# Performance work log

Measured on AMD Instinct MI355X. Metric: run time of the kernel, lower is better.

Reference implementation:

```python
import jax, jax.numpy as jnp
import numpy as np

N_NODES = 100000


def _gcn_conv(x, src, dst, deg_inv_sqrt, W, b, num_nodes):
    # GCNConv: out = D^{-1/2} (A+I) D^{-1/2} (x W) + b, with self-loops already
    # appended to (src, dst) and deg_inv_sqrt precomputed over the augmented graph.
    h = x @ W                                            # [N, out]
    coef = deg_inv_sqrt[src] * deg_inv_sqrt[dst]         # [E+N]
    msg = h[src] * coef[:, None]                         # gather + normalize
    out = jax.ops.segment_sum(msg, dst, num_segments=num_nodes)  # scatter-add
    return out + b


def setup_inputs() -> dict:
    key = jax.random.key(0)
    ks = jax.random.split(key, 8)
    n, d, h = N_NODES, 16, 16
    E = 3_200_000
    x = jax.random.normal(ks[0], (n, d), dtype=jnp.float32)
    edge_index = jax.random.randint(ks[1], (2, E), 0, n, dtype=jnp.int64)
    # Glorot-ish init for weights, zeros for biases (as in GCNConv/Linear defaults)
    W1 = jax.random.normal(ks[2], (d, h), dtype=jnp.float32) / np.sqrt(d)
    b1 = jnp.zeros((h,), dtype=jnp.float32)
    W2 = jax.random.normal(ks[3], (h, h), dtype=jnp.float32) / np.sqrt(h)
    b2 = jnp.zeros((h,), dtype=jnp.float32)
    Wfc = jax.random.normal(ks[4], (h, 1), dtype=jnp.float32) / np.sqrt(h)
    bfc = jnp.zeros((1,), dtype=jnp.float32)
    return {"x": x, "edge_index": edge_index, "W1": W1, "b1": b1,
            "W2": W2, "b2": b2, "Wfc": Wfc, "bfc": bfc}


def reference(x, edge_index, W1, b1, W2, b2, Wfc, bfc):
    n = x.shape[0]
    loops = jnp.arange(n, dtype=edge_index.dtype)
    src = jnp.concatenate([edge_index[0], loops])
    dst = jnp.concatenate([edge_index[1], loops])
    # symmetric normalization over graph with self-loops (edge weight 1)
    deg = jax.ops.segment_sum(jnp.ones_like(dst, dtype=x.dtype), dst, num_segments=n)
    deg_inv_sqrt = jnp.where(deg > 0, jax.lax.rsqrt(deg), 0.0)
    h = jax.nn.relu(_gcn_conv(x, src, dst, deg_inv_sqrt, W1, b1, n))
    h = jax.nn.relu(_gcn_conv(h, src, dst, deg_inv_sqrt, W2, b2, n))
    return h @ Wfc + bfc  # [N, 1]
```

## Files before the change

### kernel.cpp

```cpp
#include <hip/hip_runtime.h>
#include <hip/hip_fp16.h>
#include <stdint.h>


constexpr int F = 16;
constexpr int K_MAX = 256;
constexpr int BNODES = 512;
constexpr int PT = 4096;
constexpr int NPB = 128;
constexpr unsigned int CAP = 18432;

__global__ void ginit_kernel(unsigned int* __restrict__ gcur, int K) {
    int i = threadIdx.x;
    if (i < K) gcur[i] = (unsigned int)i * CAP;
}

__global__ void __launch_bounds__(256)
partition_kernel(const int* __restrict__ src, const int* __restrict__ dst,
                 unsigned int* __restrict__ gcur, unsigned int* __restrict__ recs,
                 int E, int K) {
    __shared__ unsigned int hist[K_MAX];
    __shared__ unsigned int offs[K_MAX];
    __shared__ unsigned int gbase[K_MAX];
    __shared__ unsigned int drec[PT];
    __shared__ unsigned char dbuk[PT];
    const int t = threadIdx.x;
    const int tile0 = blockIdx.x * PT;
    const int cnt = min(PT, E - tile0);
    if (t < K) hist[t] = 0u;
    __syncthreads();
    unsigned int rec[16], bp[16];
#pragma unroll
    for (int k = 0; k < 16; ++k) {
        int i = t + k * 256;
        bp[k] = 0xFFFFFFFFu;
        if (i < cnt) {
            int e = tile0 + i;
            unsigned int d = (unsigned int)dst[e];
            unsigned int s = (unsigned int)src[e];
            unsigned int b = d >> 9;
            rec[k] = ((d & 511u) << 17) | s;
            unsigned int pos = atomicAdd(&hist[b], 1u);
            bp[k] = (b << 12) | pos;
        }
    }
    __syncthreads();
    if (t < K) gbase[t] = atomicAdd(&gcur[t], hist[t]);
    if (t == 0) {
        unsigned int run = 0;
        for (int i = 0; i < K; ++i) { offs[i] = run; run += hist[i]; }
    }
    __syncthreads();
#pragma unroll
    for (int k = 0; k < 16; ++k) {
        if (bp[k] != 0xFFFFFFFFu) {
            unsigned int b = bp[k] >> 12, pos = bp[k] & 0xFFFu;
            unsigned int idx = offs[b] + pos;
            drec[idx] = rec[k];
            dbuk[idx] = (unsigned char)b;
        }
    }
    __syncthreads();
    for (int i = t; i < cnt; i += 256) {
        unsigned int b = dbuk[i];
        recs[gbase[b] + ((unsigned int)i - offs[b])] = drec[i];
    }
}

__global__ void __launch_bounds__(512)
sort_kernel(const unsigned int* __restrict__ recs, const unsigned int* __restrict__ gcur,
            float* __restrict__ dis, unsigned int* __restrict__ rp,
            unsigned int* __restrict__ recs2, int N) {
    __shared__ unsigned int cur[BNODES];
    __shared__ unsigned int wsum[8];
    const int b = blockIdx.x;
    const int t = threadIdx.x;
    const int lane = t & 63, wid = t >> 6;
    cur[t] = 0u;
    __syncthreads();
    const unsigned int e0 = (unsigned int)b * CAP;
    const unsigned int e1 = gcur[b];
    for (unsigned int e = e0 + t; e < e1; e += 512)
        atomicAdd(&cur[recs[e] >> 17], 1u);
    __syncthreads();
    const unsigned int c = cur[t];
    unsigned int x = c;
#pragma unroll
    for (int o = 1; o < 64; o <<= 1) {
        unsigned int y = __shfl_up(x, o, 64);
        if (lane >= o) x += y;
    }
    if (lane == 63) wsum[wid] = x;
    __syncthreads();
    if (t == 0) {
        unsigned int run = 0;
#pragma unroll
        for (int i = 0; i < 8; ++i) { unsigned int tmp = wsum[i]; wsum[i] = run; run += tmp; }
    }
    __syncthreads();
    const unsigned int start = e0 + wsum[wid] + x - c;
    const int v = b * BNODES + t;
    if (v < N) {
        dis[v] = rsqrtf(1.0f + (float)c);
        rp[v] = (c << 24) | start;
    }
    __syncthreads();
    cur[t] = start;
    __syncthreads();
    for (unsigned int e = e0 + t; e < e1; e += 512) {
        unsigned int r = recs[e];
        unsigned int slot = atomicAdd(&cur[r >> 17], 1u);
        recs2[slot] = r & 0x1FFFFu;
    }
}

__global__ void mv_scale_kernel(const float* __restrict__ x, const float* __restrict__ W,
                                const float* __restrict__ dis, __half* __restrict__ hs, int N) {
    __shared__ float xs[16][17];
    __shared__ float ws[16][16];
    int tid = threadIdx.x;
    int n = tid >> 4, j = tid & 15;
    int node = blockIdx.x * 16 + n;
    ws[n][j] = W[tid];
    xs[n][j] = (node < N) ? x[node * F + j] : 0.0f;
    __syncthreads();
    float acc = 0.f;
#pragma unroll
    for (int k = 0; k < 16; ++k) acc += xs[n][k] * ws[k][j];
    if (node < N) hs[node * F + j] = __float2half(acc * dis[node]);
}

__device__ __forceinline__ float2 h2f2(__half2 h) { return __half22float2(h); }

__global__ void __launch_bounds__(256)
agg1_kernel(const unsigned int* __restrict__ recs2, const unsigned int* __restrict__ rp,
            const __half2* __restrict__ hs1, const float* __restrict__ dis,
            const float* __restrict__ W2, const float* __restrict__ b1,
            __half* __restrict__ hs2, int N) {
    __shared__ float ws[16][16];
    __shared__ float hbf[NPB][17];
    const int t = threadIdx.x;
    ws[t >> 4][t & 15] = W2[t];
    const int j2 = t & 7;
    const int g8 = t >> 3;
    const int v0 = blockIdx.x * NPB;
#pragma unroll
    for (int it = 0; it < 4; ++it) {
        const int n = g8 + 32 * it;
        const int v = v0 + n;
        float sx = 0.f, sy = 0.f;
        float dv = 0.f;
        if (v < N) {
            dv = dis[v];
            const unsigned int w = rp[v];
            unsigned int e = w & 0xFFFFFFu;
            const unsigned int e1 = e + (w >> 24);
            float2 s = h2f2(hs1[(size_t)v * 8 + j2]);
            sx = s.x; sy = s.y;
            for (; e + 8 <= e1; e += 8) {
                unsigned int r0 = recs2[e + 0], r1 = recs2[e + 1];
                unsigned int r2 = recs2[e + 2], r3 = recs2[e + 3];
                unsigned int r4 = recs2[e + 4], r5 = recs2[e + 5];
                unsigned int r6 = recs2[e + 6], r7 = recs2[e + 7];
                float2 a0 = h2f2(hs1[r0 * 8 + j2]), a1 = h2f2(hs1[r1 * 8 + j2]);
                float2 a2 = h2f2(hs1[r2 * 8 + j2]), a3 = h2f2(hs1[r3 * 8 + j2]);
                float2 a4 = h2f2(hs1[r4 * 8 + j2]), a5 = h2f2(hs1[r5 * 8 + j2]);
                float2 a6 = h2f2(hs1[r6 * 8 + j2]), a7 = h2f2(hs1[r7 * 8 + j2]);
                sx += ((a0.x + a1.x) + (a2.x + a3.x)) + ((a4.x + a5.x) + (a6.x + a7.x));
                sy += ((a0.y + a1.y) + (a2.y + a3.y)) + ((a4.y + a5.y) + (a6.y + a7.y));
            }
            for (; e < e1; ++e) {
                float2 a = h2f2(hs1[recs2[e] * 8 + j2]);
                sx += a.x; sy += a.y;
            }
        }
        hbf[n][2 * j2 + 0] = fmaxf(dv * sx + b1[2 * j2 + 0], 0.f);
        hbf[n][2 * j2 + 1] = fmaxf(dv * sy + b1[2 * j2 + 1], 0.f);
    }
    __syncthreads();
    const int j = t & 15;
    const int g = t >> 4;
#pragma unroll
    for (int it = 0; it < 8; ++it) {
        const int n = g + 16 * it;
        const int v = v0 + n;
        if (v >= N) continue;
        float acc = 0.f;
#pragma unroll
        for (int k = 0; k < 16; ++k) acc += hbf[n][k] * ws[k][j];
        hs2[(size_t)v * F + j] = __float2half(acc * dis[v]);
    }
}

__global__ void __launch_bounds__(256)
agg2_kernel(const unsigned int* __restrict__ recs2, const unsigned int* __restrict__ rp,
            const __half2* __restrict__ hs2, const float* __restrict__ dis,
            const float* __restrict__ b2, const float* __restrict__ Wfc,
            const float* __restrict__ bfc, float* __restrict__ out, int N) {
    const int t = threadIdx.x;
    const int j2 = t & 7;
    const int g8 = t >> 3;
    const int v0 = blockIdx.x * NPB;
    const float wfx = Wfc[2 * j2 + 0], wfy = Wfc[2 * j2 + 1];
    const float bbx = b2[2 * j2 + 0], bby = b2[2 * j2 + 1];
    const float bf = bfc[0];
#pragma unroll
    for (int it = 0; it < 4; ++it) {
        const int v = v0 + g8 + 32 * it;
        if (v >= N) continue;
        const unsigned int w = rp[v];
        unsigned int e = w & 0xFFFFFFu;
        const unsigned int e1 = e + (w >> 24);
        float2 s0 = h2f2(hs2[(size_t)v * 8 + j2]);
        float sx = s0.x, sy = s0.y;
        for (; e + 8 <= e1; e += 8) {
            unsigned int r0 = recs2[e + 0], r1 = recs2[e + 1];
            unsigned int r2 = recs2[e + 2], r3 = recs2[e + 3];
            unsigned int r4 = recs2[e + 4], r5 = recs2[e + 5];
            unsigned int r6 = recs2[e + 6], r7 = recs2[e + 7];
            float2 a0 = h2f2(hs2[r0 * 8 + j2]), a1 = h2f2(hs2[r1 * 8 + j2]);
            float2 a2 = h2f2(hs2[r2 * 8 + j2]), a3 = h2f2(hs2[r3 * 8 + j2]);
            float2 a4 = h2f2(hs2[r4 * 8 + j2]), a5 = h2f2(hs2[r5 * 8 + j2]);
            float2 a6 = h2f2(hs2[r6 * 8 + j2]), a7 = h2f2(hs2[r7 * 8 + j2]);
            sx += ((a0.x + a1.x) + (a2.x + a3.x)) + ((a4.x + a5.x) + (a6.x + a7.x));
            sy += ((a0.y + a1.y) + (a2.y + a3.y)) + ((a4.y + a5.y) + (a6.y + a7.y));
        }
        for (; e < e1; ++e) {
            float2 a = h2f2(hs2[recs2[e] * 8 + j2]);
            sx += a.x; sy += a.y;
        }
        const float dv = dis[v];
        float h = fmaxf(dv * sx + bbx, 0.f) * wfx + fmaxf(dv * sy + bby, 0.f) * wfy;
        h += __shfl_down(h, 4, 8);
        h += __shfl_down(h, 2, 8);
        h += __shfl_down(h, 1, 8);
        if (j2 == 0) out[v] = h + bf;
    }
}

static inline char* align256(char* p) {
    return (char*)(((uintptr_t)p + 255) & ~(uintptr_t)255);
}

extern "C" void kernel_launch(void* const* d_in, const int* in_sizes, int n_in,
                              void* d_out, int out_size, void* d_ws, size_t ws_size,
                              hipStream_t stream) {
    const float* x   = (const float*)d_in[0];
    const int*   ei  = (const int*)d_in[1];
    const float* W1  = (const float*)d_in[2];
    const float* b1  = (const float*)d_in[3];
    const float* W2  = (const float*)d_in[4];
    const float* b2  = (const float*)d_in[5];
    const float* Wfc = (const float*)d_in[6];
    const float* bfc = (const float*)d_in[7];
    float* out = (float*)d_out;

    const int N = in_sizes[0] / F;
    const int E = in_sizes[1] / 2;
    const int* src = ei;
    const int* dst = ei + E;

    const int K = (N + BNODES - 1) / BNODES;

    char* p = (char*)d_ws;
    float* dis = (float*)align256(p);                   p = (char*)(dis + N);
    unsigned int* gcur  = (unsigned int*)align256(p);   p = (char*)(gcur + K);
    unsigned int* rp    = (unsigned int*)align256(p);   p = (char*)(rp + N);
    unsigned int* recs2 = (unsigned int*)align256(p);   p = (char*)(recs2 + (size_t)K * CAP);
    unsigned int* recs  = (unsigned int*)align256(p);
    __half* hs1 = (__half*)recs;
    __half* hs2 = hs1 + (size_t)N * F;

    const int T = 256;

    ginit_kernel<<<1, T, 0, stream>>>(gcur, K);
    partition_kernel<<<(E + PT - 1) / PT, T, 0, stream>>>(src, dst, gcur, recs, E, K);
    sort_kernel<<<K, 512, 0, stream>>>(recs, gcur, dis, rp, recs2, N);
    mv_scale_kernel<<<(N + 15) / 16, T, 0, stream>>>(x, W1, dis, hs1, N);
    agg1_kernel<<<(N + NPB - 1) / NPB, T, 0, stream>>>(recs2, rp, (const __half2*)hs1, dis, W2, b1, hs2, N);
    agg2_kernel<<<(N + NPB - 1) / NPB, T, 0, stream>>>(recs2, rp, (const __half2*)hs2, dis, b2, Wfc, bfc, out, N);
}
```

Before: 209.3 us.

## Fuse all GCN stages into one cooperative persistent kernel with grid syncs

Replaces the six separate launches (init, partition, sort, transform, two aggregations) with one cooperative persistent kernel that loops over tiles and separates phases with grid.sync, sharing a unioned shared-memory buffer. The partition tile is halved so each tile fits the shared-memory union under the occupancy bound. The goal is to remove launch gaps and tail effects between the small kernels. In exchange it pays for grid-wide barriers, may get lower occupancy, and the sort phase now uses 256 threads per bucket instead of 512. The old multi-kernel path remains as a fallback if the cooperative launch fails.

```diff
diff --git a/kernel.cpp b/kernel.cpp
--- a/kernel.cpp
+++ b/kernel.cpp
@@ -1,14 +1,271 @@
 #include <hip/hip_runtime.h>
 #include <hip/hip_fp16.h>
+#include <hip/hip_cooperative_groups.h>
 #include <stdint.h>
+
+namespace cg = cooperative_groups;
 
 
 constexpr int F = 16;
 constexpr int K_MAX = 256;
 constexpr int BNODES = 512;
-constexpr int PT = 4096;
+constexpr int PT = 2048;
 constexpr int NPB = 128;
 constexpr unsigned int CAP = 18432;
+
+struct SU {
+    union {
+        struct {
+            unsigned int hist[K_MAX], offs[K_MAX], gbase[K_MAX];
+            unsigned int drec[PT];
+            unsigned char dbuk[PT];
+        } part;
+        struct { unsigned int cur[BNODES]; unsigned int wsum[4]; } sort;
+        struct { float ws[16][16]; float xs[16][17]; } mv;
+        struct { float ws[16][16]; float hbf[NPB][17]; } agg;
+    };
+};
+
+__device__ __forceinline__ float2 h2f2(__half2 h) { return __half22float2(h); }
+
+__global__ void __launch_bounds__(256, 4)
+fused_kernel(const int* __restrict__ src, const int* __restrict__ dst,
+             const float* __restrict__ x,
+             const float* __restrict__ W1, const float* __restrict__ b1,
+             const float* __restrict__ W2, const float* __restrict__ b2,
+             const float* __restrict__ Wfc, const float* __restrict__ bfc,
+             float* __restrict__ out,
+             unsigned int* __restrict__ gcur, unsigned int* __restrict__ rp,
+             unsigned int* __restrict__ recs, unsigned int* __restrict__ recs2,
+             float* __restrict__ dis, __half* __restrict__ hs1, __half* __restrict__ hs2,
+             int N, int E, int K) {
+    __shared__ SU su;
+    cg::grid_group grid = cg::this_grid();
+    const int t = threadIdx.x;
+    const int blk = blockIdx.x;
+    const int nblk = gridDim.x;
+
+    {
+        int gid = blk * 256 + t;
+        if (gid < K) gcur[gid] = (unsigned int)gid * CAP;
+    }
+    grid.sync();
+
+    {
+        const int ntiles = (E + PT - 1) / PT;
+        for (int tile = blk; tile < ntiles; tile += nblk) {
+            const int tile0 = tile * PT;
+            const int cnt = min(PT, E - tile0);
+            if (t < K) su.part.hist[t] = 0u;
+            __syncthreads();
+            unsigned int rec[8], bp[8];
+#pragma unroll
+            for (int k = 0; k < 8; ++k) {
+                int i = t + k * 256;
+                bp[k] = 0xFFFFFFFFu;
+                if (i < cnt) {
+                    int e = tile0 + i;
+                    unsigned int d = (unsigned int)dst[e];
+                    unsigned int s = (unsigned int)src[e];
+                    unsigned int b = d >> 9;
+                    rec[k] = ((d & 511u) << 17) | s;
+                    unsigned int pos = atomicAdd(&su.part.hist[b], 1u);
+                    bp[k] = (b << 12) | pos;
+                }
+            }
+            __syncthreads();
+            if (t < K) su.part.gbase[t] = atomicAdd(&gcur[t], su.part.hist[t]);
+            if (t == 0) {
+                unsigned int run = 0;
+                for (int i = 0; i < K; ++i) { su.part.offs[i] = run; run += su.part.hist[i]; }
+            }
+            __syncthreads();
+#pragma unroll
+            for (int k = 0; k < 8; ++k) {
+                if (bp[k] != 0xFFFFFFFFu) {
+                    unsigned int b = bp[k] >> 12, pos = bp[k] & 0xFFFu;
+                    unsigned int idx = su.part.offs[b] + pos;
+                    su.part.drec[idx] = rec[k];
+                    su.part.dbuk[idx] = (unsigned char)b;
+                }
+            }
+            __syncthreads();
+            for (int i = t; i < cnt; i += 256) {
+                unsigned int b = su.part.dbuk[i];
+                recs[su.part.gbase[b] + ((unsigned int)i - su.part.offs[b])] = su.part.drec[i];
+            }
+            __syncthreads();
+        }
+    }
+    grid.sync();
+
+    {
+        const int lane = t & 63, wid = t >> 6;
+        for (int b = blk; b < K; b += nblk) {
+            su.sort.cur[2 * t] = 0u;
+            su.sort.cur[2 * t + 1] = 0u;
+            __syncthreads();
+            const unsigned int e0 = (unsigned int)b * CAP;
+            const unsigned int e1 = gcur[b];
+            for (unsigned int e = e0 + t; e < e1; e += 256)
+                atomicAdd(&su.sort.cur[recs[e] >> 17], 1u);
+            __syncthreads();
+            const unsigned int c0 = su.sort.cur[2 * t];
+            const unsigned int c1 = su.sort.cur[2 * t + 1];
+            const unsigned int loc = c0 + c1;
+            unsigned int xs = loc;
+#pragma unroll
+            for (int o = 1; o < 64; o <<= 1) {
+                unsigned int y = __shfl_up(xs, o, 64);
+                if (lane >= o) xs += y;
+            }
+            if (lane == 63) su.sort.wsum[wid] = xs;
+            __syncthreads();
+            if (t == 0) {
+                unsigned int run = 0;
+#pragma unroll
+                for (int i = 0; i < 4; ++i) { unsigned int tmp = su.sort.wsum[i]; su.sort.wsum[i] = run; run += tmp; }
+            }
+            __syncthreads();
+            const unsigned int start0 = e0 + su.sort.wsum[wid] + xs - loc;
+            const unsigned int start1 = start0 + c0;
+            const int v0 = b * BNODES + 2 * t;
+            if (v0 < N)     { dis[v0] = rsqrtf(1.0f + (float)c0); rp[v0] = (c0 << 24) | start0; }
+            if (v0 + 1 < N) { dis[v0 + 1] = rsqrtf(1.0f + (float)c1); rp[v0 + 1] = (c1 << 24) | start1; }
+            __syncthreads();
+            su.sort.cur[2 * t] = start0;
+            su.sort.cur[2 * t + 1] = start1;
+            __syncthreads();
+            for (unsigned int e = e0 + t; e < e1; e += 256) {
+                unsigned int r = recs[e];
+                unsigned int slot = atomicAdd(&su.sort.cur[r >> 17], 1u);
+                recs2[slot] = r & 0x1FFFFu;
+            }
+            __syncthreads();
+        }
+    }
+    grid.sync();
+
+    {
+        const int n = t >> 4, j = t & 15;
+        su.mv.ws[n][j] = W1[t];
+        __syncthreads();
+        const int ntiles = (N + 15) / 16;
+        for (int tile = blk; tile < ntiles; tile += nblk) {
+            const int node = tile * 16 + n;
+            su.mv.xs[n][j] = (node < N) ? x[node * F + j] : 0.0f;
+            __syncthreads();
+            float acc = 0.f;
+#pragma unroll
+            for (int k = 0; k < 16; ++k) acc += su.mv.xs[n][k] * su.mv.ws[k][j];
+            if (node < N) hs1[node * F + j] = __float2half(acc * dis[node]);
+            __syncthreads();
+        }
+    }
+    grid.sync();
+
+    {
+        const int j = t & 15, g = t >> 4;
+        su.agg.ws[g][j] = W2[t];
+        __syncthreads();
+        const __half2* h1 = (const __half2*)hs1;
+        const int j2 = t & 7, g8 = t >> 3;
+        const int nchunks = (N + NPB - 1) / NPB;
+        for (int chunk = blk; chunk < nchunks; chunk += nblk) {
+            const int v0 = chunk * NPB;
+#pragma unroll
+            for (int it = 0; it < 4; ++it) {
+                const int n = g8 + 32 * it;
+                const int v = v0 + n;
+                float sx = 0.f, sy = 0.f, dv = 0.f;
+                if (v < N) {
+                    dv = dis[v];
+                    const unsigned int w = rp[v];
+                    unsigned int e = w & 0xFFFFFFu;
+                    const unsigned int e1 = e + (w >> 24);
+                    float2 s = h2f2(h1[(size_t)v * 8 + j2]);
+                    sx = s.x; sy = s.y;
+                    for (; e + 8 <= e1; e += 8) {
+                        unsigned int r0 = recs2[e + 0], r1 = recs2[e + 1];
+                        unsigned int r2 = recs2[e + 2], r3 = recs2[e + 3];
+                        unsigned int r4 = recs2[e + 4], r5 = recs2[e + 5];
+                        unsigned int r6 = recs2[e + 6], r7 = recs2[e + 7];
+                        float2 a0 = h2f2(h1[r0 * 8 + j2]), a1 = h2f2(h1[r1 * 8 + j2]);
+                        float2 a2 = h2f2(h1[r2 * 8 + j2]), a3 = h2f2(h1[r3 * 8 + j2]);
+                        float2 a4 = h2f2(h1[r4 * 8 + j2]), a5 = h2f2(h1[r5 * 8 + j2]);
+                        float2 a6 = h2f2(h1[r6 * 8 + j2]), a7 = h2f2(h1[r7 * 8 + j2]);
+                        sx += ((a0.x + a1.x) + (a2.x + a3.x)) + ((a4.x + a5.x) + (a6.x + a7.x));
+                        sy += ((a0.y + a1.y) + (a2.y + a3.y)) + ((a4.y + a5.y) + (a6.y + a7.y));
+                    }
+                    for (; e < e1; ++e) {
+                        float2 a = h2f2(h1[recs2[e] * 8 + j2]);
+                        sx += a.x; sy += a.y;
+                    }
+                }
+                su.agg.hbf[n][2 * j2 + 0] = fmaxf(dv * sx + b1[2 * j2 + 0], 0.f);
+                su.agg.hbf[n][2 * j2 + 1] = fmaxf(dv * sy + b1[2 * j2 + 1], 0.f);
+            }
+            __syncthreads();
+#pragma unroll
+            for (int it = 0; it < 8; ++it) {
+                const int n = g + 16 * it;
+                const int v = v0 + n;
+                if (v < N) {
+                    float acc = 0.f;
+#pragma unroll
+                    for (int k = 0; k < 16; ++k) acc += su.agg.hbf[n][k] * su.agg.ws[k][j];
+                    hs2[(size_t)v * F + j] = __float2half(acc * dis[v]);
+                }
+            }
+            __syncthreads();
+        }
+    }
+    grid.sync();
+
+    {
+        const __half2* h2 = (const __half2*)hs2;
+        const int j2 = t & 7, g8 = t >> 3;
+        const float wfx = Wfc[2 * j2 + 0], wfy = Wfc[2 * j2 + 1];
+        const float bbx = b2[2 * j2 + 0], bby = b2[2 * j2 + 1];
+        const float bf = bfc[0];
+        const int nchunks = (N + NPB - 1) / NPB;
+        for (int chunk = blk; chunk < nchunks; chunk += nblk) {
+            const int v0 = chunk * NPB;
+#pragma unroll
+            for (int it = 0; it < 4; ++it) {
+                const int v = v0 + g8 + 32 * it;
+                if (v >= N) continue;
+                const unsigned int w = rp[v];
+                unsigned int e = w & 0xFFFFFFu;
+                const unsigned int e1 = e + (w >> 24);
+                float2 s0 = h2f2(h2[(size_t)v * 8 + j2]);
+                float sx = s0.x, sy = s0.y;
+                for (; e + 8 <= e1; e += 8) {
+                    unsigned int r0 = recs2[e + 0], r1 = recs2[e + 1];
+                    unsigned int r2 = recs2[e + 2], r3 = recs2[e + 3];
+                    unsigned int r4 = recs2[e + 4], r5 = recs2[e + 5];
+                    unsigned int r6 = recs2[e + 6], r7 = recs2[e + 7];
+                    float2 a0 = h2f2(h2[r0 * 8 + j2]), a1 = h2f2(h2[r1 * 8 + j2]);
+                    float2 a2 = h2f2(h2[r2 * 8 + j2]), a3 = h2f2(h2[r3 * 8 + j2]);
+                    float2 a4 = h2f2(h2[r4 * 8 + j2]), a5 = h2f2(h2[r5 * 8 + j2]);
+                    float2 a6 = h2f2(h2[r6 * 8 + j2]), a7 = h2f2(h2[r7 * 8 + j2]);
+                    sx += ((a0.x + a1.x) + (a2.x + a3.x)) + ((a4.x + a5.x) + (a6.x + a7.x));
+                    sy += ((a0.y + a1.y) + (a2.y + a3.y)) + ((a4.y + a5.y) + (a6.y + a7.y));
+                }
+                for (; e < e1; ++e) {
+                    float2 a = h2f2(h2[recs2[e] * 8 + j2]);
+                    sx += a.x; sy += a.y;
+                }
+                const float dv = dis[v];
+                float h = fmaxf(dv * sx + bbx, 0.f) * wfx + fmaxf(dv * sy + bby, 0.f) * wfy;
+                h += __shfl_down(h, 4, 8);
+                h += __shfl_down(h, 2, 8);
+                h += __shfl_down(h, 1, 8);
+                if (j2 == 0) out[v] = h + bf;
+            }
+        }
+    }
+}
 
 __global__ void ginit_kernel(unsigned int* __restrict__ gcur, int K) {
     int i = threadIdx.x;
@@ -29,9 +286,9 @@
     const int cnt = min(PT, E - tile0);
     if (t < K) hist[t] = 0u;
     __syncthreads();
-    unsigned int rec[16], bp[16];
-#pragma unroll
-    for (int k = 0; k < 16; ++k) {
+    unsigned int rec[8], bp[8];
+#pragma unroll
+    for (int k = 0; k < 8; ++k) {
         int i = t + k * 256;
         bp[k] = 0xFFFFFFFFu;
         if (i < cnt) {
@@ -52,7 +309,7 @@
     }
     __syncthreads();
 #pragma unroll
-    for (int k = 0; k < 16; ++k) {
+    for (int k = 0; k < 8; ++k) {
         if (bp[k] != 0xFFFFFFFFu) {
             unsigned int b = bp[k] >> 12, pos = bp[k] & 0xFFFu;
             unsigned int idx = offs[b] + pos;
@@ -129,8 +386,6 @@
     for (int k = 0; k < 16; ++k) acc += xs[n][k] * ws[k][j];
     if (node < N) hs[node * F + j] = __float2half(acc * dis[node]);
 }
-
-__device__ __forceinline__ float2 h2f2(__half2 h) { return __half22float2(h); }
 
 __global__ void __launch_bounds__(256)
 agg1_kernel(const unsigned int* __restrict__ recs2, const unsigned int* __restrict__ rp,
@@ -148,8 +403,7 @@
     for (int it = 0; it < 4; ++it) {
         const int n = g8 + 32 * it;
         const int v = v0 + n;
-        float sx = 0.f, sy = 0.f;
-        float dv = 0.f;
+        float sx = 0.f, sy = 0.f, dv = 0.f;
         if (v < N) {
             dv = dis[v];
             const unsigned int w = rp[v];
@@ -255,12 +509,11 @@
     const float* bfc = (const float*)d_in[7];
     float* out = (float*)d_out;
 
-    const int N = in_sizes[0] / F;
-    const int E = in_sizes[1] / 2;
+    int N = in_sizes[0] / F;
+    int E = in_sizes[1] / 2;
     const int* src = ei;
     const int* dst = ei + E;
-
-    const int K = (N + BNODES - 1) / BNODES;
+    int K = (N + BNODES - 1) / BNODES;
 
     char* p = (char*)d_ws;
     float* dis = (float*)align256(p);                   p = (char*)(dis + N);
@@ -271,12 +524,24 @@
     __half* hs1 = (__half*)recs;
     __half* hs2 = hs1 + (size_t)N * F;
 
-    const int T = 256;
-
-    ginit_kernel<<<1, T, 0, stream>>>(gcur, K);
-    partition_kernel<<<(E + PT - 1) / PT, T, 0, stream>>>(src, dst, gcur, recs, E, K);
-    sort_kernel<<<K, 512, 0, stream>>>(recs, gcur, dis, rp, recs2, N);
-    mv_scale_kernel<<<(N + 15) / 16, T, 0, stream>>>(x, W1, dis, hs1, N);
-    agg1_kernel<<<(N + NPB - 1) / NPB, T, 0, stream>>>(recs2, rp, (const __half2*)hs1, dis, W2, b1, hs2, N);
-    agg2_kernel<<<(N + NPB - 1) / NPB, T, 0, stream>>>(recs2, rp, (const __half2*)hs2, dis, b2, Wfc, bfc, out, N);
-}
+    int nb = 0;
+    hipError_t qerr = hipOccupancyMaxActiveBlocksPerMultiprocessor(
+        &nb, (const void*)fused_kernel, 256, 0);
+    hipError_t lerr = hipErrorUnknown;
+    if (qerr == hipSuccess && nb > 0) {
+        int grid = nb * 256;
+        void* args[] = { &src, &dst, &x, &W1, &b1, &W2, &b2, &Wfc, &bfc, &out,
+                         &gcur, &rp, &recs, &recs2, &dis, &hs1, &hs2, &N, &E, &K };
+        lerr = hipLaunchCooperativeKernel((void*)fused_kernel, dim3(grid),
+                                          dim3(256), args, 0, stream);
+    }
+    if (lerr != hipSuccess) {
+        const int T = 256;
+        ginit_kernel<<<1, T, 0, stream>>>(gcur, K);
+        partition_kernel<<<(E + PT - 1) / PT, T, 0, stream>>>(src, dst, gcur, recs, E, K);
+        sort_kernel<<<K, 512, 0, stream>>>(recs, gcur, dis, rp, recs2, N);
+        mv_scale_kernel<<<(N + 15) / 16, T, 0, stream>>>(x, W1, dis, hs1, N);
+        agg1_kernel<<<(N + NPB - 1) / NPB, T, 0, stream>>>(recs2, rp, (const __half2*)hs1, dis, W2, b1, hs2, N);
+        agg2_kernel<<<(N + NPB - 1) / NPB, T, 0, stream>>>(recs2, rp, (const __half2*)hs2, dis, b2, Wfc, bfc, out, N);
+    }
+}
```

After: 650.4 us. 211% more time.

## Fuse first-layer matvec into sort kernel and shrink aggregation node blocks

Applied to the files above, without the earlier changes.

Folds the first-layer x·W1 scaled by the degree norm into the per-bucket sort kernel, reusing the degree values already in shared memory, so a separate launch and its dis reread go away. The gcur init kernel becomes a memset, with the bucket base offset added inside the partition and sort kernels. The aggregation kernels now handle 32 nodes per block instead of 128, giving more blocks and better load balance for the irregular gather. hs1/hs2 get their own buffers instead of aliasing recs. The sort blocks do more serial work, and smaller agg blocks lose per-block reuse of the W2 load.

```diff
diff --git a/kernel.cpp b/kernel.cpp
--- a/kernel.cpp
+++ b/kernel.cpp
@@ -7,13 +7,10 @@
 constexpr int K_MAX = 256;
 constexpr int BNODES = 512;
 constexpr int PT = 4096;
-constexpr int NPB = 128;
+constexpr int NPB = 32;
 constexpr unsigned int CAP = 18432;
 
-__global__ void ginit_kernel(unsigned int* __restrict__ gcur, int K) {
-    int i = threadIdx.x;
-    if (i < K) gcur[i] = (unsigned int)i * CAP;
-}
+__device__ __forceinline__ float2 h2f2(__half2 h) { return __half22float2(h); }
 
 __global__ void __launch_bounds__(256)
 partition_kernel(const int* __restrict__ src, const int* __restrict__ dst,
@@ -45,7 +42,7 @@
         }
     }
     __syncthreads();
-    if (t < K) gbase[t] = atomicAdd(&gcur[t], hist[t]);
+    if (t < K) gbase[t] = (unsigned int)t * CAP + atomicAdd(&gcur[t], hist[t]);
     if (t == 0) {
         unsigned int run = 0;
         for (int i = 0; i < K; ++i) { offs[i] = run; run += hist[i]; }
@@ -68,29 +65,34 @@
 }
 
 __global__ void __launch_bounds__(512)
-sort_kernel(const unsigned int* __restrict__ recs, const unsigned int* __restrict__ gcur,
-            float* __restrict__ dis, unsigned int* __restrict__ rp,
-            unsigned int* __restrict__ recs2, int N) {
+sort_mv_kernel(const unsigned int* __restrict__ recs, const unsigned int* __restrict__ gcur,
+               const float* __restrict__ x, const float* __restrict__ W1,
+               float* __restrict__ dis, unsigned int* __restrict__ rp,
+               unsigned int* __restrict__ recs2, __half* __restrict__ hs1, int N) {
     __shared__ unsigned int cur[BNODES];
     __shared__ unsigned int wsum[8];
+    __shared__ float sdis[BNODES];
+    __shared__ float ws[16][16];
+    __shared__ float xs[32][17];
     const int b = blockIdx.x;
     const int t = threadIdx.x;
     const int lane = t & 63, wid = t >> 6;
     cur[t] = 0u;
+    if (t < 256) ws[t >> 4][t & 15] = W1[t];
     __syncthreads();
     const unsigned int e0 = (unsigned int)b * CAP;
-    const unsigned int e1 = gcur[b];
+    const unsigned int e1 = e0 + gcur[b];
     for (unsigned int e = e0 + t; e < e1; e += 512)
         atomicAdd(&cur[recs[e] >> 17], 1u);
     __syncthreads();
     const unsigned int c = cur[t];
-    unsigned int x = c;
+    unsigned int xsc = c;
 #pragma unroll
     for (int o = 1; o < 64; o <<= 1) {
-        unsigned int y = __shfl_up(x, o, 64);
-        if (lane >= o) x += y;
-    }
-    if (lane == 63) wsum[wid] = x;
+        unsigned int y = __shfl_up(xsc, o, 64);
+        if (lane >= o) xsc += y;
+    }
+    if (lane == 63) wsum[wid] = xsc;
     __syncthreads();
     if (t == 0) {
         unsigned int run = 0;
@@ -98,10 +100,12 @@
         for (int i = 0; i < 8; ++i) { unsigned int tmp = wsum[i]; wsum[i] = run; run += tmp; }
     }
     __syncthreads();
-    const unsigned int start = e0 + wsum[wid] + x - c;
+    const unsigned int start = e0 + wsum[wid] + xsc - c;
     const int v = b * BNODES + t;
+    const float dv = rsqrtf(1.0f + (float)c);
+    sdis[t] = dv;
     if (v < N) {
-        dis[v] = rsqrtf(1.0f + (float)c);
+        dis[v] = dv;
         rp[v] = (c << 24) | start;
     }
     __syncthreads();
@@ -112,25 +116,20 @@
         unsigned int slot = atomicAdd(&cur[r >> 17], 1u);
         recs2[slot] = r & 0x1FFFFu;
     }
-}
-
-__global__ void mv_scale_kernel(const float* __restrict__ x, const float* __restrict__ W,
-                                const float* __restrict__ dis, __half* __restrict__ hs, int N) {
-    __shared__ float xs[16][17];
-    __shared__ float ws[16][16];
-    int tid = threadIdx.x;
-    int n = tid >> 4, j = tid & 15;
-    int node = blockIdx.x * 16 + n;
-    ws[n][j] = W[tid];
-    xs[n][j] = (node < N) ? x[node * F + j] : 0.0f;
-    __syncthreads();
-    float acc = 0.f;
-#pragma unroll
-    for (int k = 0; k < 16; ++k) acc += xs[n][k] * ws[k][j];
-    if (node < N) hs[node * F + j] = __float2half(acc * dis[node]);
-}
-
-__device__ __forceinline__ float2 h2f2(__half2 h) { return __half22float2(h); }
+    const int n = t >> 4, j = t & 15;
+#pragma unroll
+    for (int tile = 0; tile < 16; ++tile) {
+        const int loc = tile * 32 + n;
+        const int node = b * BNODES + loc;
+        __syncthreads();
+        xs[n][j] = (node < N) ? x[(size_t)node * F + j] : 0.0f;
+        __syncthreads();
+        float acc = 0.f;
+#pragma unroll
+        for (int k = 0; k < 16; ++k) acc += xs[n][k] * ws[k][j];
+        if (node < N) hs1[(size_t)node * F + j] = __float2half(acc * sdis[loc]);
+    }
+}
 
 __global__ void __launch_bounds__(256)
 agg1_kernel(const unsigned int* __restrict__ recs2, const unsigned int* __restrict__ rp,
@@ -144,12 +143,9 @@
     const int j2 = t & 7;
     const int g8 = t >> 3;
     const int v0 = blockIdx.x * NPB;
-#pragma unroll
-    for (int it = 0; it < 4; ++it) {
-        const int n = g8 + 32 * it;
-        const int v = v0 + n;
-        float sx = 0.f, sy = 0.f;
-        float dv = 0.f;
+    {
+        const int v = v0 + g8;
+        float sx = 0.f, sy = 0.f, dv = 0.f;
         if (v < N) {
             dv = dis[v];
             const unsigned int w = rp[v];
@@ -174,14 +170,14 @@
                 sx += a.x; sy += a.y;
             }
         }
-        hbf[n][2 * j2 + 0] = fmaxf(dv * sx + b1[2 * j2 + 0], 0.f);
-        hbf[n][2 * j2 + 1] = fmaxf(dv * sy + b1[2 * j2 + 1], 0.f);
+        hbf[g8][2 * j2 + 0] = fmaxf(dv * sx + b1[2 * j2 + 0], 0.f);
+        hbf[g8][2 * j2 + 1] = fmaxf(dv * sy + b1[2 * j2 + 1], 0.f);
     }
     __syncthreads();
     const int j = t & 15;
     const int g = t >> 4;
 #pragma unroll
-    for (int it = 0; it < 8; ++it) {
+    for (int it = 0; it < 2; ++it) {
         const int n = g + 16 * it;
         const int v = v0 + n;
         if (v >= N) continue;
@@ -204,38 +200,35 @@
     const float wfx = Wfc[2 * j2 + 0], wfy = Wfc[2 * j2 + 1];
     const float bbx = b2[2 * j2 + 0], bby = b2[2 * j2 + 1];
     const float bf = bfc[0];
-#pragma unroll
-    for (int it = 0; it < 4; ++it) {
-        const int v = v0 + g8 + 32 * it;
-        if (v >= N) continue;
-        const unsigned int w = rp[v];
-        unsigned int e = w & 0xFFFFFFu;
-        const unsigned int e1 = e + (w >> 24);
-        float2 s0 = h2f2(hs2[(size_t)v * 8 + j2]);
-        float sx = s0.x, sy = s0.y;
-        for (; e + 8 <= e1; e += 8) {
-            unsigned int r0 = recs2[e + 0], r1 = recs2[e + 1];
-            unsigned int r2 = recs2[e + 2], r3 = recs2[e + 3];
-            unsigned int r4 = recs2[e + 4], r5 = recs2[e + 5];
-            unsigned int r6 = recs2[e + 6], r7 = recs2[e + 7];
-            float2 a0 = h2f2(hs2[r0 * 8 + j2]), a1 = h2f2(hs2[r1 * 8 + j2]);
-            float2 a2 = h2f2(hs2[r2 * 8 + j2]), a3 = h2f2(hs2[r3 * 8 + j2]);
-            float2 a4 = h2f2(hs2[r4 * 8 + j2]), a5 = h2f2(hs2[r5 * 8 + j2]);
-            float2 a6 = h2f2(hs2[r6 * 8 + j2]), a7 = h2f2(hs2[r7 * 8 + j2]);
-            sx += ((a0.x + a1.x) + (a2.x + a3.x)) + ((a4.x + a5.x) + (a6.x + a7.x));
-            sy += ((a0.y + a1.y) + (a2.y + a3.y)) + ((a4.y + a5.y) + (a6.y + a7.y));
-        }
-        for (; e < e1; ++e) {
-            float2 a = h2f2(hs2[recs2[e] * 8 + j2]);
-            sx += a.x; sy += a.y;
-        }
-        const float dv = dis[v];
-        float h = fmaxf(dv * sx + bbx, 0.f) * wfx + fmaxf(dv * sy + bby, 0.f) * wfy;
-        h += __shfl_down(h, 4, 8);
-        h += __shfl_down(h, 2, 8);
-        h += __shfl_down(h, 1, 8);
-        if (j2 == 0) out[v] = h + bf;
-    }
+    const int v = v0 + g8;
+    if (v >= N) return;
+    const unsigned int w = rp[v];
+    unsigned int e = w & 0xFFFFFFu;
+    const unsigned int e1 = e + (w >> 24);
+    float2 s0 = h2f2(hs2[(size_t)v * 8 + j2]);
+    float sx = s0.x, sy = s0.y;
+    for (; e + 8 <= e1; e += 8) {
+        unsigned int r0 = recs2[e + 0], r1 = recs2[e + 1];
+        unsigned int r2 = recs2[e + 2], r3 = recs2[e + 3];
+        unsigned int r4 = recs2[e + 4], r5 = recs2[e + 5];
+        unsigned int r6 = recs2[e + 6], r7 = recs2[e + 7];
+        float2 a0 = h2f2(hs2[r0 * 8 + j2]), a1 = h2f2(hs2[r1 * 8 + j2]);
+        float2 a2 = h2f2(hs2[r2 * 8 + j2]), a3 = h2f2(hs2[r3 * 8 + j2]);
+        float2 a4 = h2f2(hs2[r4 * 8 + j2]), a5 = h2f2(hs2[r5 * 8 + j2]);
+        float2 a6 = h2f2(hs2[r6 * 8 + j2]), a7 = h2f2(hs2[r7 * 8 + j2]);
+        sx += ((a0.x + a1.x) + (a2.x + a3.x)) + ((a4.x + a5.x) + (a6.x + a7.x));
+        sy += ((a0.y + a1.y) + (a2.y + a3.y)) + ((a4.y + a5.y) + (a6.y + a7.y));
+    }
+    for (; e < e1; ++e) {
+        float2 a = h2f2(hs2[recs2[e] * 8 + j2]);
+        sx += a.x; sy += a.y;
+    }
+    const float dv = dis[v];
+    float h = fmaxf(dv * sx + bbx, 0.f) * wfx + fmaxf(dv * sy + bby, 0.f) * wfy;
+    h += __shfl_down(h, 4, 8);
+    h += __shfl_down(h, 2, 8);
+    h += __shfl_down(h, 1, 8);
+    if (j2 == 0) out[v] = h + bf;
 }
 
 static inline char* align256(char* p) {
@@ -259,7 +252,6 @@
     const int E = in_sizes[1] / 2;
     const int* src = ei;
     const int* dst = ei + E;
-
     const int K = (N + BNODES - 1) / BNODES;
 
     char* p = (char*)d_ws;
@@ -267,16 +259,15 @@
     unsigned int* gcur  = (unsigned int*)align256(p);   p = (char*)(gcur + K);
     unsigned int* rp    = (unsigned int*)align256(p);   p = (char*)(rp + N);
     unsigned int* recs2 = (unsigned int*)align256(p);   p = (char*)(recs2 + (size_t)K * CAP);
-    unsigned int* recs  = (unsigned int*)align256(p);
-    __half* hs1 = (__half*)recs;
-    __half* hs2 = hs1 + (size_t)N * F;
+    unsigned int* recs  = (unsigned int*)align256(p);   p = (char*)(recs + (size_t)K * CAP);
+    __half* hs1 = (__half*)align256(p);                 p = (char*)(hs1 + (size_t)N * F);
+    __half* hs2 = (__half*)align256(p);
 
     const int T = 256;
 
-    ginit_kernel<<<1, T, 0, stream>>>(gcur, K);
+    hipMemsetAsync(gcur, 0, (size_t)K * sizeof(unsigned int), stream);
     partition_kernel<<<(E + PT - 1) / PT, T, 0, stream>>>(src, dst, gcur, recs, E, K);
-    sort_kernel<<<K, 512, 0, stream>>>(recs, gcur, dis, rp, recs2, N);
-    mv_scale_kernel<<<(N + 15) / 16, T, 0, stream>>>(x, W1, dis, hs1, N);
+    sort_mv_kernel<<<K, 512, 0, stream>>>(recs, gcur, x, W1, dis, rp, recs2, hs1, N);
     agg1_kernel<<<(N + NPB - 1) / NPB, T, 0, stream>>>(recs2, rp, (const __half2*)hs1, dis, W2, b1, hs2, N);
     agg2_kernel<<<(N + NPB - 1) / NPB, T, 0, stream>>>(recs2, rp, (const __half2*)hs2, dis, b2, Wfc, bfc, out, N);
 }
```

Measured after the change: 197.1 us. -5.9%, faster.
